# Optimization experiments

Hardware: AMD Instinct MI355X
Metric: run time of the kernel (lower is better)

## Reference

```python
import jax, jax.numpy as jnp
import numpy as np

N, E, IN, H, C, B, DD = 50000, 800000, 128, 4, 32, 64, 32
HC = H * C  # 128 = hidden_dim * num_heads


def setup_inputs() -> dict:
    key = jax.random.key(0)
    ks = jax.random.split(key, 28)
    r = lambda i, shape: jax.random.normal(ks[i], shape, jnp.float32) * 0.05
    return {
        "x": jax.random.normal(ks[0], (N, IN), jnp.float32),
        "domain": jax.random.normal(ks[1], (B, DD), jnp.float32),
        "Wl1": r(2, (HC, IN)), "bl1": r(3, (HC,)),
        "Wr1": r(4, (HC, IN)), "br1": r(5, (HC,)),
        "att1": r(6, (H, C)), "bias1": r(7, (HC,)),
        "Wl2": r(8, (HC, HC)), "bl2": r(9, (HC,)),
        "Wr2": r(10, (HC, HC)), "br2": r(11, (HC,)),
        "att2": r(12, (H, C)), "bias2": r(13, (HC,)),
        "Wres": r(14, (HC, IN)), "bres": r(15, (HC,)),
        "Wd": r(16, (64, DD)), "bd": r(17, (64,)),
        "Wg": r(18, (HC, HC)), "bg": r(19, (HC,)),
        "Wf1": r(20, (128, HC + 64)), "bf1": r(21, (128,)),
        "Wf2": r(22, (64, 128)), "bf2": r(23, (64,)),
        "Wf3": r(24, (1, 64)), "bf3": r(25, (1,)),
        "edge_index": jax.random.randint(ks[26], (2, E), 0, N),
        "batch": jnp.sort(jax.random.randint(ks[27], (N,), 0, B)),
    }


def gatv2_conv(x, src, dst, Wl, bl, Wr, br, att, bias):
    """PyG GATv2Conv, add_self_loops=False, concat heads, eval (no dropout)."""
    n = x.shape[0]
    xl = (x @ Wl.T + bl).reshape(n, H, C)  # source-side transform (lin_l)
    xr = (x @ Wr.T + br).reshape(n, H, C)  # target-side transform (lin_r)
    e = jax.nn.leaky_relu(xl[src] + xr[dst], 0.2)            # [E,H,C]
    s = jnp.einsum('ehc,hc->eh', e, att)                      # [E,H]
    smax = jax.ops.segment_max(s, dst, num_segments=n)        # per-dst max
    a = jnp.exp(s - smax[dst])
    denom = jax.ops.segment_sum(a, dst, num_segments=n)
    alpha = a / denom[dst]                                    # segment softmax
    out = jax.ops.segment_sum(alpha[:, :, None] * xl[src], dst, num_segments=n)
    return out.reshape(n, HC) + bias


def reference(x, domain, Wl1, bl1, Wr1, br1, att1, bias1,
              Wl2, bl2, Wr2, br2, att2, bias2,
              Wres, bres, Wd, bd, Wg, bg,
              Wf1, bf1, Wf2, bf2, Wf3, bf3,
              edge_index, batch):
    src, dst = edge_index[0], edge_index[1]
    res = x @ Wres.T + bres
    h = jax.nn.relu(gatv2_conv(x, src, dst, Wl1, bl1, Wr1, br1, att1, bias1)) + res
    h = jax.nn.relu(gatv2_conv(h, src, dst, Wl2, bl2, Wr2, br2, att2, bias2)) + h
    # global mean pool over graphs
    sums = jax.ops.segment_sum(h, batch, num_segments=B)
    counts = jax.ops.segment_sum(jnp.ones((h.shape[0],), h.dtype), batch, num_segments=B)
    pooled = sums / jnp.maximum(counts, 1.0)[:, None]
    g = jax.nn.relu(pooled @ Wg.T + bg)
    d = jax.nn.relu(domain @ Wd.T + bd)
    z = jnp.concatenate([g, d], axis=1)
    z = jax.nn.relu(z @ Wf1.T + bf1)
    z = jax.nn.relu(z @ Wf2.T + bf2)
    return (z @ Wf3.T + bf3).squeeze()
```

## Files before the change

kernel.cpp:

```cpp
#include <hip/hip_runtime.h>
#include <math.h>

#define NN 50000
#define NE 800000
#define FD 128
#define NB 64
#define NBUK 196
#define CHK 3125
#define CAP 6144
#define NBLK 782

typedef __attribute__((ext_vector_type(8))) short short8v;
typedef __attribute__((ext_vector_type(4))) float f32x4;
typedef _Float16 h2 __attribute__((ext_vector_type(2)));
typedef _Float16 h8 __attribute__((ext_vector_type(8)));

__device__ __forceinline__ unsigned short f2h(float f) {
  return __builtin_bit_cast(unsigned short, (_Float16)f);
}
__device__ __forceinline__ float h2f(unsigned short u) {
  return (float)__builtin_bit_cast(_Float16, u);
}

__device__ __forceinline__ size_t img_base(int n, int lane) {
  int lrow = n & 63, blk = n >> 6;
  int kh = lane >> 4, s7 = (lane >> 1) & 7, off4 = (lane & 1) * 4;
  return (size_t)blk * 8192 + kh * 4096 + lrow * 64 + 8 * (s7 ^ (lrow & 7)) + off4;
}

__global__ __launch_bounds__(256) void k_prep1(const float* __restrict__ W0,
    const float* __restrict__ W1, const float* __restrict__ W2,
    const float* __restrict__ W3, const float* __restrict__ W4,
    unsigned short* __restrict__ wh, unsigned short* __restrict__ wl,
    const int* __restrict__ dst, int* __restrict__ bcnt) {
  __shared__ int bh[NBUK];
  int bx = blockIdx.x;
  if (bx < 40) {
    int id = bx * 256 + threadIdx.x;
    if (id >= 5 * 2048) return;
    int w = id >> 11, rem = id & 2047;
    int row = rem >> 4, slot = rem & 15;
    const float* Wp = (w == 0) ? W0 : (w == 1) ? W1 : (w == 2) ? W2 : (w == 3) ? W3 : W4;
    const float* sp = &Wp[row * 128 + slot * 8];
    int kh = slot >> 3, s7 = slot & 7;
    int d = ((w * 2 + kh) * 8192) + row * 64 + 8 * (s7 ^ (row & 7));
    short8v hi, lo;
    #pragma unroll
    for (int j = 0; j < 8; ++j) {
      float f = sp[j];
      _Float16 hv = (_Float16)f;
      _Float16 lv = (_Float16)(f - (float)hv);
      hi[j] = (short)__builtin_bit_cast(unsigned short, hv);
      lo[j] = (short)__builtin_bit_cast(unsigned short, lv);
    }
    *(short8v*)&wh[d] = hi;
    *(short8v*)&wl[d] = lo;
  } else {
    int b = bx - 40;
    int t = threadIdx.x;
    for (int i = t; i < NBUK; i += 256) bh[i] = 0;
    __syncthreads();
    int e0 = b * CHK, e1 = e0 + CHK;
    if (e1 > NE) e1 = NE;
    for (int e = e0 + t; e < e1; e += 256) atomicAdd(&bh[dst[e] >> 8], 1);
    __syncthreads();
    for (int i = t; i < NBUK; i += 256) if (bh[i]) atomicAdd(&bcnt[i], bh[i]);
  }
}

__global__ __launch_bounds__(256) void k_bscan(const int* __restrict__ bcnt,
                                               int* __restrict__ bbase,
                                               int* __restrict__ bcur) {
  __shared__ int wsum[4];
  int t = threadIdx.x;
  int v = (t < NBUK) ? bcnt[t] : 0;
  int lane = t & 63, wv = t >> 6;
  int s = v;
  #pragma unroll
  for (int off = 1; off < 64; off <<= 1) {
    int y = __shfl_up(s, off, 64);
    if (lane >= off) s += y;
  }
  if (lane == 63) wsum[wv] = s;
  __syncthreads();
  if (t == 0) {
    int r = 0;
    #pragma unroll
    for (int i = 0; i < 4; ++i) { int x = wsum[i]; wsum[i] = r; r += x; }
  }
  __syncthreads();
  int excl = s - v + wsum[wv];
  if (t < NBUK) { bbase[t] = excl; bcur[t] = excl; }
  if (t == NBUK - 1) bbase[NBUK] = excl + v;
}

__global__ __launch_bounds__(256) void k_prep2(const float* __restrict__ x,
    unsigned short* __restrict__ ximg,
    const int* __restrict__ src, const int* __restrict__ dst,
    int* __restrict__ bcur, int* __restrict__ tmpv) {
  __shared__ int bh[NBUK];
  __shared__ int bb[NBUK];
  __shared__ int brun[NBUK];
  int bx = blockIdx.x;
  if (bx < 3125) {
    int id = bx * 256 + threadIdx.x;
    int row = id >> 4, slot = id & 15;
    const float* sp = &x[(size_t)row * 128 + slot * 8];
    int blk = row >> 6, lrow = row & 63, kh = slot >> 3, s7 = slot & 7;
    size_t hoff = (size_t)blk * 8192 + kh * 4096 + lrow * 64 + 8 * (s7 ^ (lrow & 7));
    short8v hv;
    #pragma unroll
    for (int j = 0; j < 8; ++j)
      hv[j] = (short)f2h(sp[j]);
    *(short8v*)&ximg[hoff] = hv;
  } else {
    int b = bx - 3125;
    int t = threadIdx.x;
    int e0 = b * CHK, e1 = e0 + CHK;
    if (e1 > NE) e1 = NE;
    for (int i = t; i < NBUK; i += 256) { bh[i] = 0; brun[i] = 0; }
    __syncthreads();
    for (int e = e0 + t; e < e1; e += 256) atomicAdd(&bh[dst[e] >> 8], 1);
    __syncthreads();
    for (int i = t; i < NBUK; i += 256)
      bb[i] = bh[i] ? atomicAdd(&bcur[i], bh[i]) : 0;
    __syncthreads();
    for (int e = e0 + t; e < e1; e += 256) {
      int d = dst[e];
      int bk = d >> 8;
      int p = bb[bk] + atomicAdd(&brun[bk], 1);
      tmpv[p] = (src[e] << 8) | (d & 255);
    }
  }
}

__device__ __forceinline__ void linm2_body(
    const unsigned short* __restrict__ aimg,
    const unsigned short* __restrict__ wh_img, const unsigned short* __restrict__ wl_img,
    int wimg, const float* __restrict__ bias,
    _Float16* __restrict__ out_h, int blk, char* smem) {
  unsigned short* s_a  = (unsigned short*)smem;
  unsigned short* s_wh = s_a + 4096;
  unsigned short* s_wl = s_wh + 8192;
  const int tid = threadIdx.x;
  const int lane = tid & 63;
  const int wv = tid >> 6;
  const int m0 = (wv >> 2) * 32;
  const int n0 = (wv & 3) * 32;
  const int rbase = blk * 64;
  const int g = lane >> 4, lr = lane & 15;

  f32x4 acc[2][2];
  #pragma unroll
  for (int mt = 0; mt < 2; ++mt)
    #pragma unroll
    for (int nt = 0; nt < 2; ++nt)
      acc[mt][nt] = (f32x4){0.f, 0.f, 0.f, 0.f};

  for (int kh = 0; kh < 2; ++kh) {
    if (kh) __syncthreads();
    {
      const short8v* asrc = (const short8v*)(aimg + (size_t)blk * 8192 + kh * 4096);
      ((short8v*)s_a)[tid] = asrc[tid];
    }
    {
      const short8v* whs = (const short8v*)(wh_img + (size_t)(wimg * 2 + kh) * 8192);
      const short8v* wls = (const short8v*)(wl_img + (size_t)(wimg * 2 + kh) * 8192);
      short8v* whd = (short8v*)s_wh;
      short8v* wld = (short8v*)s_wl;
      whd[tid] = whs[tid]; whd[512 + tid] = whs[512 + tid];
      wld[tid] = wls[tid]; wld[512 + tid] = wls[512 + tid];
    }
    __syncthreads();
    #pragma unroll
    for (int ks = 0; ks < 2; ++ks) {
      const int slot = ks * 4 + g;
      h8 a[2];
      #pragma unroll
      for (int mt = 0; mt < 2; ++mt) {
        int row = m0 + mt * 16 + lr;
        int idx = row * 64 + 8 * (slot ^ (row & 7));
        a[mt] = __builtin_bit_cast(h8, *(const short8v*)&s_a[idx]);
      }
      #pragma unroll
      for (int nt = 0; nt < 2; ++nt) {
        int row2 = n0 + nt * 16 + lr;
        int idx2 = row2 * 64 + 8 * (slot ^ (row2 & 7));
        h8 bh = __builtin_bit_cast(h8, *(const short8v*)&s_wh[idx2]);
        h8 bl = __builtin_bit_cast(h8, *(const short8v*)&s_wl[idx2]);
        #pragma unroll
        for (int mt = 0; mt < 2; ++mt) {
          acc[mt][nt] = __builtin_amdgcn_mfma_f32_16x16x32_f16(a[mt], bh, acc[mt][nt], 0, 0, 0);
          acc[mt][nt] = __builtin_amdgcn_mfma_f32_16x16x32_f16(a[mt], bl, acc[mt][nt], 0, 0, 0);
        }
      }
    }
  }
  #pragma unroll
  for (int nt = 0; nt < 2; ++nt) {
    float bv = bias[n0 + nt * 16 + lr];
    #pragma unroll
    for (int mt = 0; mt < 2; ++mt)
      #pragma unroll
      for (int i = 0; i < 4; ++i) {
        int r = rbase + m0 + mt * 16 + 4 * g + i;
        if (r < NN) {
          float vv = acc[mt][nt][i] + bv;
          out_h[(size_t)r * 128 + n0 + nt * 16 + lr] = (_Float16)vv;
        }
      }
  }
}

__global__ __launch_bounds__(512, 8) void k_csrlin(
    const int* __restrict__ tmpv, const int* __restrict__ bbase,
    int* __restrict__ offs, int* __restrict__ ssrc,
    const unsigned short* __restrict__ ximg,
    const unsigned short* __restrict__ wh_img, const unsigned short* __restrict__ wl_img,
    const float* __restrict__ bl1, const float* __restrict__ br1, const float* __restrict__ bres,
    _Float16* __restrict__ xl, _Float16* __restrict__ xr,
    _Float16* __restrict__ res) {
  __shared__ __align__(16) char smem[40960];
  int bx = blockIdx.x;
  if (bx < NBUK) {
    int* sdeg = (int*)smem;
    int* scur = sdeg + 256;
    int* wsum = scur + 256;
    int* lsrc = wsum + 16;
    int b = bx, t = threadIdx.x;
    int es = bbase[b], ee = bbase[b + 1];
    int cnt = ee - es;
    if (t < 256) sdeg[t] = 0;
    __syncthreads();
    for (int i = t; i < cnt; i += 512) atomicAdd(&sdeg[tmpv[es + i] & 255], 1);
    __syncthreads();
    int v = 0, s = 0;
    int lane = t & 63, wv = t >> 6;
    if (t < 256) {
      v = sdeg[t];
      s = v;
      #pragma unroll
      for (int off = 1; off < 64; off <<= 1) {
        int y = __shfl_up(s, off, 64);
        if (lane >= off) s += y;
      }
      if (lane == 63) wsum[wv] = s;
    }
    __syncthreads();
    if (t == 0) {
      int r = 0;
      #pragma unroll
      for (int i = 0; i < 4; ++i) { int x2 = wsum[i]; wsum[i] = r; r += x2; }
    }
    __syncthreads();
    if (t < 256) {
      int excl = s - v + wsum[wv];
      scur[t] = excl;
      int node = b * 256 + t;
      if (node < NN) offs[node] = es + excl;
    }
    if (b == 0 && t == 0) offs[NN] = NE;
    __syncthreads();
    if (cnt <= CAP) {
      for (int i = t; i < cnt; i += 512) {
        int pkt = tmpv[es + i];
        int p = atomicAdd(&scur[pkt & 255], 1);
        lsrc[p] = pkt >> 8;
      }
      __syncthreads();
      for (int i = t; i < cnt; i += 512) ssrc[es + i] = lsrc[i];
    } else {
      for (int i = t; i < cnt; i += 512) {
        int pkt = tmpv[es + i];
        int p = atomicAdd(&scur[pkt & 255], 1);
        ssrc[es + p] = pkt >> 8;
      }
    }
  } else {
    int bf = bx - NBUK;
    int w = bf / NBLK, blk = bf % NBLK;
    const float* bias = (w == 0) ? bl1 : (w == 1) ? br1 : bres;
    _Float16* oh = (w == 0) ? xl : (w == 1) ? xr : res;
    linm2_body(ximg, wh_img, wl_img, w, bias, oh, blk, smem);
  }
}

__global__ __launch_bounds__(512, 8) void k_lin2(
    const unsigned short* __restrict__ himg,
    const unsigned short* __restrict__ wh_img, const unsigned short* __restrict__ wl_img,
    const float* __restrict__ bl2, const float* __restrict__ br2,
    _Float16* __restrict__ xl, _Float16* __restrict__ xr) {
  __shared__ __align__(16) char smem[40960];
  int w = blockIdx.y;
  linm2_body(himg, wh_img, wl_img, 3 + w, (w == 0) ? bl2 : br2,
             (w == 0) ? xl : xr, blockIdx.x, smem);
}

__device__ __forceinline__ float4 gat_core(const _Float16* __restrict__ xl,
    const _Float16* __restrict__ xr, const int* __restrict__ offs,
    const int* __restrict__ ssrc, const float* __restrict__ att,
    const float* __restrict__ bias, int n, int lane) {
  float4 att4 = ((const float4*)att)[lane];
  h2 att01 = {(_Float16)att4.x, (_Float16)att4.y};
  h2 att23 = {(_Float16)att4.z, (_Float16)att4.w};
  uint2 xru = ((const uint2*)xr)[(size_t)n * 32 + lane];
  h2 xr01 = __builtin_bit_cast(h2, xru.x);
  h2 xr23 = __builtin_bit_cast(h2, xru.y);
  const h2 k02 = {(_Float16)0.2f, (_Float16)0.2f};
  int e0 = offs[n], e1 = offs[n + 1];
  float den = 0.f;
  float4 acc = make_float4(0.f, 0.f, 0.f, 0.f);
  int e = e0;
  for (; e + 3 < e1; e += 4) {
    uint2 u[4];
    #pragma unroll
    for (int j = 0; j < 4; ++j) {
      int s = ssrc[e + j];
      u[j] = ((const uint2*)xl)[(size_t)s * 32 + lane];
    }
    #pragma unroll
    for (int j = 0; j < 4; ++j) {
      h2 v01 = __builtin_bit_cast(h2, u[j].x);
      h2 v23 = __builtin_bit_cast(h2, u[j].y);
      h2 t01 = v01 + xr01;
      h2 t23 = v23 + xr23;
      h2 l01 = __builtin_elementwise_max(t01, t01 * k02);
      h2 l23 = __builtin_elementwise_max(t23, t23 * k02);
      float p = __builtin_amdgcn_fdot2(l01, att01, 0.f, false);
      p = __builtin_amdgcn_fdot2(l23, att23, p, false);
      p += __shfl_xor(p, 1, 64); p += __shfl_xor(p, 2, 64); p += __shfl_xor(p, 4, 64);
      float w = __expf(p);
      den += w;
      acc.x += w * (float)v01[0];
      acc.y += w * (float)v01[1];
      acc.z += w * (float)v23[0];
      acc.w += w * (float)v23[1];
    }
  }
  for (; e < e1; ++e) {
    int s = ssrc[e];
    uint2 uu = ((const uint2*)xl)[(size_t)s * 32 + lane];
    h2 v01 = __builtin_bit_cast(h2, uu.x);
    h2 v23 = __builtin_bit_cast(h2, uu.y);
    h2 t01 = v01 + xr01;
    h2 t23 = v23 + xr23;
    h2 l01 = __builtin_elementwise_max(t01, t01 * k02);
    h2 l23 = __builtin_elementwise_max(t23, t23 * k02);
    float p = __builtin_amdgcn_fdot2(l01, att01, 0.f, false);
    p = __builtin_amdgcn_fdot2(l23, att23, p, false);
    p += __shfl_xor(p, 1, 64); p += __shfl_xor(p, 2, 64); p += __shfl_xor(p, 4, 64);
    float w = __expf(p);
    den += w;
    acc.x += w * (float)v01[0];
    acc.y += w * (float)v01[1];
    acc.z += w * (float)v23[0];
    acc.w += w * (float)v23[1];
  }
  float inv = (den > 0.f) ? 1.f / den : 0.f;
  float4 b4 = ((const float4*)bias)[lane];
  float4 o;
  o.x = fmaxf(acc.x * inv + b4.x, 0.f);
  o.y = fmaxf(acc.y * inv + b4.y, 0.f);
  o.z = fmaxf(acc.z * inv + b4.z, 0.f);
  o.w = fmaxf(acc.w * inv + b4.w, 0.f);
  return o;
}

__global__ __launch_bounds__(256) void k_gat1(const _Float16* __restrict__ xl,
    const _Float16* __restrict__ xr, const int* __restrict__ offs,
    const int* __restrict__ ssrc, const float* __restrict__ att,
    const float* __restrict__ bias, const _Float16* __restrict__ resid,
    unsigned short* __restrict__ himg) {
  int grp = threadIdx.x >> 5;
  int lane = threadIdx.x & 31;
  int n = blockIdx.x * 8 + grp;
  float4 o = gat_core(xl, xr, offs, ssrc, att, bias, n, lane);
  uint2 ru = ((const uint2*)resid)[(size_t)n * 32 + lane];
  h2 r01 = __builtin_bit_cast(h2, ru.x);
  h2 r23 = __builtin_bit_cast(h2, ru.y);
  o.x += (float)r01[0]; o.y += (float)r01[1];
  o.z += (float)r23[0]; o.w += (float)r23[1];
  size_t base = img_base(n, lane);
  ushort4 hv;
  hv.x = f2h(o.x); hv.y = f2h(o.y); hv.z = f2h(o.z); hv.w = f2h(o.w);
  *(ushort4*)&himg[base] = hv;
}

__global__ __launch_bounds__(256) void k_gatpool(const _Float16* __restrict__ xl,
    const _Float16* __restrict__ xr, const int* __restrict__ offs,
    const int* __restrict__ ssrc, const float* __restrict__ att,
    const float* __restrict__ bias, const unsigned short* __restrict__ himg,
    const int* __restrict__ batch, float* __restrict__ pooled) {
  __shared__ float sm[8][128];
  __shared__ int sbat[8];
  int grp = threadIdx.x >> 5;
  int lane = threadIdx.x & 31;
  int n = blockIdx.x * 8 + grp;
  float4 o = gat_core(xl, xr, offs, ssrc, att, bias, n, lane);
  size_t base = img_base(n, lane);
  ushort4 rh = *(const ushort4*)&himg[base];
  o.x += h2f(rh.x); o.y += h2f(rh.y); o.z += h2f(rh.z); o.w += h2f(rh.w);
  *(float4*)&sm[grp][lane * 4] = o;
  if (threadIdx.x < 8) sbat[threadIdx.x] = batch[blockIdx.x * 8 + threadIdx.x];
  __syncthreads();
  int t = threadIdx.x;
  if (t < 128) {
    float run = sm[0][t];
    int cb = sbat[0];
    #pragma unroll
    for (int g2 = 1; g2 < 8; ++g2) {
      int bb = sbat[g2];
      if (bb != cb) { atomicAdd(&pooled[cb * FD + t], run); run = 0.f; cb = bb; }
      run += sm[g2][t];
    }
    atomicAdd(&pooled[cb * FD + t], run);
  }
}

__global__ __launch_bounds__(128) void k_mlp(const float* __restrict__ pooled,
    const int* __restrict__ batch, const float* __restrict__ domain,
    const float* __restrict__ Wg, const float* __restrict__ bg,
    const float* __restrict__ Wd, const float* __restrict__ bd,
    const float* __restrict__ Wf1, const float* __restrict__ bf1,
    const float* __restrict__ Wf2, const float* __restrict__ bf2,
    const float* __restrict__ Wf3, const float* __restrict__ bf3,
    float* __restrict__ out) {
  __shared__ float z[192];
  __shared__ float z1[128];
  __shared__ float z2[64];
  __shared__ float pm[128];
  __shared__ int cnt;
  int b = blockIdx.x, t = threadIdx.x;
  if (t == 0) {
    int lo = 0, hi = NN;
    while (lo < hi) { int mid = (lo + hi) >> 1; if (batch[mid] < b) lo = mid + 1; else hi = mid; }
    int lb = lo; lo = 0; hi = NN;
    while (lo < hi) { int mid = (lo + hi) >> 1; if (batch[mid] < b + 1) lo = mid + 1; else hi = mid; }
    cnt = lo - lb;
  }
  __syncthreads();
  float invc = 1.f / fmaxf((float)cnt, 1.f);
  pm[t] = pooled[b * FD + t] * invc;
  __syncthreads();
  {
    float a = bg[t];
    for (int k = 0; k < 128; ++k) a += pm[k] * Wg[t * 128 + k];
    z[t] = fmaxf(a, 0.f);
  }
  if (t < 64) {
    float a = bd[t];
    for (int k = 0; k < 32; ++k) a += domain[b * 32 + k] * Wd[t * 32 + k];
    z[128 + t] = fmaxf(a, 0.f);
  }
  __syncthreads();
  {
    float a = bf1[t];
    for (int k = 0; k < 192; ++k) a += z[k] * Wf1[t * 192 + k];
    z1[t] = fmaxf(a, 0.f);
  }
  __syncthreads();
  if (t < 64) {
    float a = bf2[t];
    for (int k = 0; k < 128; ++k) a += z1[k] * Wf2[t * 128 + k];
    z2[t] = fmaxf(a, 0.f);
  }
  __syncthreads();
  if (t < 64) {
    float v = z2[t] * Wf3[t];
    for (int off = 1; off < 64; off <<= 1) v += __shfl_xor(v, off, 64);
    if (t == 0) out[b] = v + bf3[0];
  }
}

extern "C" void kernel_launch(void* const* d_in, const int* in_sizes, int n_in,
                              void* d_out, int out_size, void* d_ws, size_t ws_size,
                              hipStream_t stream) {
  const float* x      = (const float*)d_in[0];
  const float* domain = (const float*)d_in[1];
  const float* Wl1 = (const float*)d_in[2];  const float* bl1 = (const float*)d_in[3];
  const float* Wr1 = (const float*)d_in[4];  const float* br1 = (const float*)d_in[5];
  const float* att1= (const float*)d_in[6];  const float* bias1=(const float*)d_in[7];
  const float* Wl2 = (const float*)d_in[8];  const float* bl2 = (const float*)d_in[9];
  const float* Wr2 = (const float*)d_in[10]; const float* br2 = (const float*)d_in[11];
  const float* att2= (const float*)d_in[12]; const float* bias2=(const float*)d_in[13];
  const float* Wres= (const float*)d_in[14]; const float* bres= (const float*)d_in[15];
  const float* Wd  = (const float*)d_in[16]; const float* bd  = (const float*)d_in[17];
  const float* Wg  = (const float*)d_in[18]; const float* bg  = (const float*)d_in[19];
  const float* Wf1 = (const float*)d_in[20]; const float* bf1 = (const float*)d_in[21];
  const float* Wf2 = (const float*)d_in[22]; const float* bf2 = (const float*)d_in[23];
  const float* Wf3 = (const float*)d_in[24]; const float* bf3 = (const float*)d_in[25];
  const int* ei    = (const int*)d_in[26];
  const int* batch = (const int*)d_in[27];
  const int* esrc = ei;
  const int* edst = ei + NE;
  float* outp = (float*)d_out;

  char* p = (char*)d_ws;
  auto carve = [&](size_t bytes) { char* r = p; p += (bytes + 255) & ~(size_t)255; return r; };
  int* bcnt     = (int*)carve((size_t)NBUK * 4);
  int* bbase    = (int*)carve((size_t)(NBUK + 1) * 4);
  int* bcur     = (int*)carve((size_t)NBUK * 4);
  int* tmpv     = (int*)carve((size_t)NE * 4);
  int* ssrc     = (int*)carve((size_t)NE * 4);
  int* offs     = (int*)carve((size_t)(NN + 1) * 4);
  unsigned short* wh = (unsigned short*)carve((size_t)5 * 2 * 8192 * 2);
  unsigned short* wl = (unsigned short*)carve((size_t)5 * 2 * 8192 * 2);
  unsigned short* ximg = (unsigned short*)carve((size_t)NBLK * 8192 * 2);
  _Float16* xl  = (_Float16*)carve((size_t)NN * FD * 2);
  _Float16* xr  = (_Float16*)carve((size_t)NN * FD * 2);
  _Float16* res = (_Float16*)carve((size_t)NN * FD * 2);
  float* pooled = (float*)carve((size_t)NB * FD * 4);
  unsigned short* himg = ximg;

  hipMemsetAsync(bcnt, 0, (size_t)NBUK * 4, stream);
  hipMemsetAsync(pooled, 0, (size_t)NB * FD * 4, stream);

  dim3 b256(256);
  hipLaunchKernelGGL(k_prep1, dim3(40 + 256), b256, 0, stream,
                     Wl1, Wr1, Wres, Wl2, Wr2, wh, wl, edst, bcnt);
  hipLaunchKernelGGL(k_bscan, dim3(1), b256, 0, stream, bcnt, bbase, bcur);
  hipLaunchKernelGGL(k_prep2, dim3(3125 + 256), b256, 0, stream,
                     x, ximg, esrc, edst, bcur, tmpv);
  hipLaunchKernelGGL(k_csrlin, dim3(NBUK + 3 * NBLK), dim3(512), 0, stream,
                     tmpv, bbase, offs, ssrc, ximg, wh, wl, bl1, br1, bres, xl, xr, res);
  hipLaunchKernelGGL(k_gat1, dim3(NN / 8), b256, 0, stream,
                     xl, xr, offs, ssrc, att1, bias1, res, himg);
  hipLaunchKernelGGL(k_lin2, dim3(NBLK, 2), dim3(512), 0, stream,
                     himg, wh, wl, bl2, br2, xl, xr);
  hipLaunchKernelGGL(k_gatpool, dim3(NN / 8), b256, 0, stream,
                     xl, xr, offs, ssrc, att2, bias2, himg, batch, pooled);
  hipLaunchKernelGGL(k_mlp, dim3(NB), dim3(128), 0, stream, pooled, batch, domain,
                     Wg, bg, Wd, bd, Wf1, bf1, Wf2, bf2, Wf3, bf3, outp);
}
```

Measured before the change: 185.5 us.

## Move x fp16 conversion into prep1 and split edge scatter into finer blocks

Moves the x-to-fp16 swizzled image conversion from the second prep kernel into the first, so it runs alongside bucket counting and weight prep. The scatter then becomes a kernel of its own with 1024 blocks of 782 edges each instead of 256 blocks of 3125. The aim is to take the conversion work off the critical path behind the scan and to spread the scatter across more blocks for better occupancy. In exchange there are more global atomics on the bucket cursors, and the order of edges within a bucket changes.

```diff
diff --git a/kernel.cpp b/kernel.cpp
--- a/kernel.cpp
+++ b/kernel.cpp
@@ -7,6 +7,8 @@
 #define NB 64
 #define NBUK 196
 #define CHK 3125
+#define NSC 1024
+#define CHK2 782
 #define CAP 6144
 #define NBLK 782
 
@@ -32,11 +34,21 @@
     const float* __restrict__ W1, const float* __restrict__ W2,
     const float* __restrict__ W3, const float* __restrict__ W4,
     unsigned short* __restrict__ wh, unsigned short* __restrict__ wl,
-    const int* __restrict__ dst, int* __restrict__ bcnt) {
+    const int* __restrict__ dst, int* __restrict__ bcnt,
+    const float* __restrict__ x, unsigned short* __restrict__ ximg) {
   __shared__ int bh[NBUK];
   int bx = blockIdx.x;
-  if (bx < 40) {
-    int id = bx * 256 + threadIdx.x;
+  if (bx < 256) {
+    int t = threadIdx.x;
+    for (int i = t; i < NBUK; i += 256) bh[i] = 0;
+    __syncthreads();
+    int e0 = bx * CHK, e1 = e0 + CHK;
+    if (e1 > NE) e1 = NE;
+    for (int e = e0 + t; e < e1; e += 256) atomicAdd(&bh[dst[e] >> 8], 1);
+    __syncthreads();
+    for (int i = t; i < NBUK; i += 256) if (bh[i]) atomicAdd(&bcnt[i], bh[i]);
+  } else if (bx < 296) {
+    int id = (bx - 256) * 256 + threadIdx.x;
     if (id >= 5 * 2048) return;
     int w = id >> 11, rem = id & 2047;
     int row = rem >> 4, slot = rem & 15;
@@ -56,15 +68,16 @@
     *(short8v*)&wh[d] = hi;
     *(short8v*)&wl[d] = lo;
   } else {
-    int b = bx - 40;
-    int t = threadIdx.x;
-    for (int i = t; i < NBUK; i += 256) bh[i] = 0;
-    __syncthreads();
-    int e0 = b * CHK, e1 = e0 + CHK;
-    if (e1 > NE) e1 = NE;
-    for (int e = e0 + t; e < e1; e += 256) atomicAdd(&bh[dst[e] >> 8], 1);
-    __syncthreads();
-    for (int i = t; i < NBUK; i += 256) if (bh[i]) atomicAdd(&bcnt[i], bh[i]);
+    int id = (bx - 296) * 256 + threadIdx.x;
+    int row = id >> 4, slot = id & 15;
+    const float* sp = &x[(size_t)row * 128 + slot * 8];
+    int blk = row >> 6, lrow = row & 63, kh = slot >> 3, s7 = slot & 7;
+    size_t hoff = (size_t)blk * 8192 + kh * 4096 + lrow * 64 + 8 * (s7 ^ (lrow & 7));
+    short8v hv;
+    #pragma unroll
+    for (int j = 0; j < 8; ++j)
+      hv[j] = (short)f2h(sp[j]);
+    *(short8v*)&ximg[hoff] = hv;
   }
 }
 
@@ -94,43 +107,26 @@
   if (t == NBUK - 1) bbase[NBUK] = excl + v;
 }
 
-__global__ __launch_bounds__(256) void k_prep2(const float* __restrict__ x,
-    unsigned short* __restrict__ ximg,
-    const int* __restrict__ src, const int* __restrict__ dst,
-    int* __restrict__ bcur, int* __restrict__ tmpv) {
+__global__ __launch_bounds__(256) void k_bscatter(const int* __restrict__ src,
+    const int* __restrict__ dst, int* __restrict__ bcur, int* __restrict__ tmpv) {
   __shared__ int bh[NBUK];
   __shared__ int bb[NBUK];
   __shared__ int brun[NBUK];
-  int bx = blockIdx.x;
-  if (bx < 3125) {
-    int id = bx * 256 + threadIdx.x;
-    int row = id >> 4, slot = id & 15;
-    const float* sp = &x[(size_t)row * 128 + slot * 8];
-    int blk = row >> 6, lrow = row & 63, kh = slot >> 3, s7 = slot & 7;
-    size_t hoff = (size_t)blk * 8192 + kh * 4096 + lrow * 64 + 8 * (s7 ^ (lrow & 7));
-    short8v hv;
-    #pragma unroll
-    for (int j = 0; j < 8; ++j)
-      hv[j] = (short)f2h(sp[j]);
-    *(short8v*)&ximg[hoff] = hv;
-  } else {
-    int b = bx - 3125;
-    int t = threadIdx.x;
-    int e0 = b * CHK, e1 = e0 + CHK;
-    if (e1 > NE) e1 = NE;
-    for (int i = t; i < NBUK; i += 256) { bh[i] = 0; brun[i] = 0; }
-    __syncthreads();
-    for (int e = e0 + t; e < e1; e += 256) atomicAdd(&bh[dst[e] >> 8], 1);
-    __syncthreads();
-    for (int i = t; i < NBUK; i += 256)
-      bb[i] = bh[i] ? atomicAdd(&bcur[i], bh[i]) : 0;
-    __syncthreads();
-    for (int e = e0 + t; e < e1; e += 256) {
-      int d = dst[e];
-      int bk = d >> 8;
-      int p = bb[bk] + atomicAdd(&brun[bk], 1);
-      tmpv[p] = (src[e] << 8) | (d & 255);
-    }
+  int t = threadIdx.x;
+  int e0 = blockIdx.x * CHK2, e1 = e0 + CHK2;
+  if (e1 > NE) e1 = NE;
+  for (int i = t; i < NBUK; i += 256) { bh[i] = 0; brun[i] = 0; }
+  __syncthreads();
+  for (int e = e0 + t; e < e1; e += 256) atomicAdd(&bh[dst[e] >> 8], 1);
+  __syncthreads();
+  for (int i = t; i < NBUK; i += 256)
+    bb[i] = bh[i] ? atomicAdd(&bcur[i], bh[i]) : 0;
+  __syncthreads();
+  for (int e = e0 + t; e < e1; e += 256) {
+    int d = dst[e];
+    int bk = d >> 8;
+    int p = bb[bk] + atomicAdd(&brun[bk], 1);
+    tmpv[p] = (src[e] << 8) | (d & 255);
   }
 }
 
@@ -516,11 +512,10 @@
   hipMemsetAsync(pooled, 0, (size_t)NB * FD * 4, stream);
 
   dim3 b256(256);
-  hipLaunchKernelGGL(k_prep1, dim3(40 + 256), b256, 0, stream,
-                     Wl1, Wr1, Wres, Wl2, Wr2, wh, wl, edst, bcnt);
+  hipLaunchKernelGGL(k_prep1, dim3(256 + 40 + 3125), b256, 0, stream,
+                     Wl1, Wr1, Wres, Wl2, Wr2, wh, wl, edst, bcnt, x, ximg);
   hipLaunchKernelGGL(k_bscan, dim3(1), b256, 0, stream, bcnt, bbase, bcur);
-  hipLaunchKernelGGL(k_prep2, dim3(3125 + 256), b256, 0, stream,
-                     x, ximg, esrc, edst, bcur, tmpv);
+  hipLaunchKernelGGL(k_bscatter, dim3(NSC), b256, 0, stream, esrc, edst, bcur, tmpv);
   hipLaunchKernelGGL(k_csrlin, dim3(NBUK + 3 * NBLK), dim3(512), 0, stream,
                      tmpv, bbase, offs, ssrc, ximg, wh, wl, bl1, br1, bres, xl, xr, res);
   hipLaunchKernelGGL(k_gat1, dim3(NN / 8), b256, 0, stream,
```

After: 186.6 us. No clear change (+0.6%).
